# Kernel optimization log

Measured on AMD Instinct MI355X. Metric: run time of the kernel, lower is better.

The kernel has to match this reference:

```python
import jax, jax.numpy as jnp
import numpy as np

EPS_L2 = 1e-6   # featureL2Norm epsilon
EPS_MM = 1e-5   # MutualMatching epsilon
K_POOL = 2      # relocalization_k_size


def feature_l2norm(f):
    # torch: f / sqrt(sum(f^2, dim=1) + eps)
    norm = jnp.sqrt(jnp.sum(f * f, axis=1, keepdims=True) + EPS_L2)
    return f / norm


def mutual_matching(c):
    # c: [b, 1, f1, f2, f3, f4]
    b_max = jnp.max(c, axis=(2, 3), keepdims=True)  # max over source positions
    a_max = jnp.max(c, axis=(4, 5), keepdims=True)  # max over target positions
    return c * (c / (a_max + EPS_MM)) * (c / (b_max + EPS_MM))


def maxpool4d_max(c, k):
    # c: [b, 1, H, W, H2, W2] -> strided 4D max pool (max over all k^4 offsets)
    b = c.shape[0]
    H, W, H2, W2 = c.shape[2:]
    x = c[:, 0].reshape(b, H // k, k, W // k, k, H2 // k, k, W2 // k, k)
    x = x.transpose(0, 1, 3, 5, 7, 2, 4, 6, 8)
    x = x.reshape(b, H // k, W // k, H2 // k, W2 // k, k ** 4)
    return jnp.max(x, axis=-1)[:, None]  # [b,1,H/k,W/k,H2/k,W2/k]


def conv4d(x, w, b):
    # x: [N, Cin, d1, d2, d3, d4], w: [Cout, Cin, 3,3,3,3], SAME padding (pre-pad 1)
    y = jax.lax.conv_general_dilated(x, w, window_strides=(1, 1, 1, 1), padding='SAME')
    return y + b.reshape(1, -1, 1, 1, 1, 1)


def setup_inputs() -> dict:
    key = jax.random.key(0)
    ks = jax.random.split(key, 8)
    B, C, H, W = 8, 1024, 48, 48
    return {
        'feature_A': jax.random.normal(ks[0], (B, C, H, W), dtype=jnp.float32),
        'feature_B': jax.random.normal(ks[1], (B, C, H, W), dtype=jnp.float32),
        'w1': jax.random.normal(ks[2], (10, 1, 3, 3, 3, 3), dtype=jnp.float32) * 0.05,
        'b1': jnp.zeros((10,), dtype=jnp.float32),
        'w2': jax.random.normal(ks[3], (10, 10, 3, 3, 3, 3), dtype=jnp.float32) * 0.05,
        'b2': jnp.zeros((10,), dtype=jnp.float32),
        'w3': jax.random.normal(ks[4], (1, 10, 3, 3, 3, 3), dtype=jnp.float32) * 0.05,
        'b3': jnp.zeros((1,), dtype=jnp.float32),
    }


def reference(feature_A, feature_B, w1, b1, w2, b2, w3, b3):
    # 1) L2-normalize features over channels
    fa = feature_l2norm(feature_A)
    fb = feature_l2norm(feature_B)
    b, c, h, w = fa.shape
    # 2) 4D correlation: [b, hA*wA, hB*wB]
    corr = jnp.einsum('bcp,bcq->bpq', fa.reshape(b, c, h * w), fb.reshape(b, c, h * w))
    corr = corr.reshape(b, 1, h, w, h, w)
    # ReLU + featureL2Norm over singleton channel dim => x / sqrt(x^2 + eps)
    corr = jax.nn.relu(corr)
    corr = corr / jnp.sqrt(corr * corr + EPS_L2)
    # 3) strided 4D max pool (relocalization)
    corr = maxpool4d_max(corr, K_POOL)
    # 4) mutual matching
    corr = mutual_matching(corr)
    x = jax.nn.relu(conv4d(corr, w1, b1))
    x = jax.nn.relu(conv4d(x, w2, b2))
    x = jax.nn.relu(conv4d(x, w3, b3))
    # 6) mutual matching again
    return mutual_matching(x)
```

## Files before the change

kernel.cpp:

```cpp
#include <hip/hip_runtime.h>
#include <hip/hip_bf16.h>
#include <math.h>

#define C_   1024
#define P_   2304
#define S4   331776

typedef __attribute__((ext_vector_type(8))) short short8;
typedef __attribute__((ext_vector_type(4))) float f32x4;
typedef __attribute__((ext_vector_type(4))) unsigned int u32x4;

__device__ inline unsigned short f2bf(float v) {
  unsigned u = __builtin_bit_cast(unsigned, v);
  u += 0x7fffu + ((u >> 16) & 1u);
  return (unsigned short)(u >> 16);
}
__device__ inline float bf2f(unsigned short h) {
  unsigned u = ((unsigned)h) << 16;
  return __builtin_bit_cast(float, u);
}

__device__ inline void async16(const void* g, void* l) {
  __builtin_amdgcn_global_load_lds(
      (const __attribute__((address_space(1))) unsigned int*)g,
      (__attribute__((address_space(3))) unsigned int*)l, 16, 0, 0);
}

__global__ __launch_bounds__(256) void k_prep(
    const float* __restrict__ fA, const float* __restrict__ fB,
    unsigned short* __restrict__ TAhi, unsigned short* __restrict__ TAlo,
    unsigned short* __restrict__ TBhi, unsigned short* __restrict__ TBlo,
    float* __restrict__ part) {
  __shared__ float ld[64 * 65];
  __shared__ float pslds[512];
  const int c0 = blockIdx.x * 64, p0 = blockIdx.y * 64;
  const int fb = blockIdx.z, f = fb >> 3, b = fb & 7;
  const float* src = (f ? fB : fA) + (size_t)b * C_ * P_;
  unsigned short* Thi = (f ? TBhi : TAhi) + (size_t)b * P_ * C_;
  unsigned short* Tlo = (f ? TBlo : TAlo) + (size_t)b * P_ * C_;
  const int t = threadIdx.x;
#pragma unroll
  for (int e = 0; e < 4; ++e) {
    int cid = t + e * 256;
    int r = cid >> 4, ch = cid & 15;
    float4 v = *(const float4*)&src[(size_t)(c0 + r) * P_ + p0 + ch * 4];
    ld[r * 65 + ch * 4 + 0] = v.x;
    ld[r * 65 + ch * 4 + 1] = v.y;
    ld[r * 65 + ch * 4 + 2] = v.z;
    ld[r * 65 + ch * 4 + 3] = v.w;
  }
  __syncthreads();
#pragma unroll
  for (int e = 0; e < 2; ++e) {
    int ocid = t + e * 256;
    int pl = ocid >> 3, c8 = ocid & 7;
    unsigned short hi[8], lo[8];
    float sq = 0.f;
#pragma unroll
    for (int s = 0; s < 8; ++s) {
      float v = ld[(c8 * 8 + s) * 65 + pl];
      unsigned short h = f2bf(v);
      float rem = v - bf2f(h);
      hi[s] = h; lo[s] = f2bf(rem);
      sq = fmaf(v, v, sq);
    }
    size_t go = (size_t)(p0 + pl) * C_ + c0 + c8 * 8;
    *(uint4*)&Thi[go] = *(uint4*)hi;
    *(uint4*)&Tlo[go] = *(uint4*)lo;
    pslds[ocid] = sq;
  }
  __syncthreads();
  if (t < 64) {
    float s = 0.f;
#pragma unroll
    for (int c8 = 0; c8 < 8; ++c8) s += pslds[t * 8 + c8];
    part[((size_t)fb * 16 + blockIdx.x) * P_ + p0 + t] = s;
  }
}

__global__ void k_invnorm(const float* __restrict__ part, float* __restrict__ inv) {
  int p = blockIdx.x * 256 + threadIdx.x;
  int fb = blockIdx.y;
  float s = 1e-6f;
  for (int ct = 0; ct < 16; ++ct) s += part[((size_t)fb * 16 + ct) * P_ + p];
  inv[(size_t)fb * P_ + p] = 1.0f / sqrtf(s);
}

__global__ __launch_bounds__(256, 3) void k_corr_mfma(
    const unsigned short* __restrict__ TAhi_, const unsigned short* __restrict__ TAlo_,
    const unsigned short* __restrict__ TBhi_, const unsigned short* __restrict__ TBlo_,
    const float* __restrict__ invn, float* __restrict__ pooled) {
  __shared__ __align__(16) char lds_raw[37248];
  unsigned short* stage = (unsigned short*)lds_raw;
  float* epi = (float*)lds_raw;

  const int b = blockIdx.y;
  const size_t tb = (size_t)b * P_ * C_;
  const unsigned short* TAhi = TAhi_ + tb;
  const unsigned short* TAlo = TAlo_ + tb;
  const unsigned short* TBhi = TBhi_ + tb;
  const unsigned short* TBlo = TBlo_ + tb;
  float* out = pooled + (size_t)b * S4;

  const int g = blockIdx.x;
  const int xcd = g & 7, idx = g >> 3;
  const int ti = (xcd & 3) * 6 + idx % 6;
  const int tj = (xcd >> 2) * 12 + idx / 6;
  const int p0 = ti * 96, q0 = tj * 96;
  const int t = threadIdx.x;
  const int lane = t & 63, w = t >> 6;
  const int wr = w >> 1, wc = w & 1;
  const int m15 = lane & 15, q4 = lane >> 4;
  const int koff = q4 * 8;

  f32x4 acc[3][3];
#pragma unroll
  for (int a = 0; a < 3; ++a)
#pragma unroll
    for (int c = 0; c < 3; ++c) acc[a][c] = (f32x4){0.f, 0.f, 0.f, 0.f};

  const unsigned short* gld[8];
  int ldsb[8];
#pragma unroll
  for (int e = 0; e < 8; ++e) {
    int chunk = (w * 8 + e) * 64 + lane;
    int arr = chunk / 480;
    int rem = chunk - arr * 480;
    int row = rem / 5, kc = rem - row * 5;
    bool dum = (arr >= 4) || (kc == 4);
    if (arr >= 4) { arr = 0; row = 0; }
    const unsigned short* base = (arr == 0) ? TAhi : (arr == 1) ? TAlo
                               : (arr == 2) ? TBhi : TBlo;
    int pb = (arr < 2) ? p0 : q0;
    gld[e] = base + (size_t)(pb + row) * C_ + (dum ? 0 : kc * 8);
    ldsb[e] = (w * 8 + e) * 1024;
  }

  for (int kt = 0; kt < C_; kt += 32) {
    __syncthreads();
#pragma unroll
    for (int e = 0; e < 8; ++e)
      async16(gld[e] + kt, lds_raw + ldsb[e]);
    asm volatile("s_waitcnt vmcnt(0)" ::: "memory");
    __syncthreads();

    const unsigned short* Ah = stage;
    const unsigned short* Al = stage + 3840;
    const unsigned short* Bh = stage + 7680;
    const unsigned short* Bl = stage + 11520;
    short8 ah[3], al[3], bh[3], bl[3];
#pragma unroll
    for (int a = 0; a < 3; ++a) {
      int row = wr * 48 + a * 16 + m15;
      ah[a] = *(const short8*)&Ah[row * 40 + koff];
      al[a] = *(const short8*)&Al[row * 40 + koff];
    }
#pragma unroll
    for (int c = 0; c < 3; ++c) {
      int row = wc * 48 + c * 16 + m15;
      bh[c] = *(const short8*)&Bh[row * 40 + koff];
      bl[c] = *(const short8*)&Bl[row * 40 + koff];
    }
#pragma unroll
    for (int a = 0; a < 3; ++a)
#pragma unroll
      for (int c = 0; c < 3; ++c)
        acc[a][c] = __builtin_amdgcn_mfma_f32_16x16x32_bf16(ah[a], bh[c], acc[a][c], 0, 0, 0);
#pragma unroll
    for (int a = 0; a < 3; ++a)
#pragma unroll
      for (int c = 0; c < 3; ++c)
        acc[a][c] = __builtin_amdgcn_mfma_f32_16x16x32_bf16(ah[a], bl[c], acc[a][c], 0, 0, 0);
#pragma unroll
    for (int a = 0; a < 3; ++a)
#pragma unroll
      for (int c = 0; c < 3; ++c)
        acc[a][c] = __builtin_amdgcn_mfma_f32_16x16x32_bf16(al[a], bh[c], acc[a][c], 0, 0, 0);
  }
  __syncthreads();

  const float* invA = invn + (size_t)b * P_;
  const float* invB = invn + (size_t)(8 + b) * P_;
  float ib[3];
#pragma unroll
  for (int c = 0; c < 3; ++c) ib[c] = invB[q0 + wc * 48 + c * 16 + m15];
#pragma unroll
  for (int a = 0; a < 3; ++a) {
#pragma unroll
    for (int reg = 0; reg < 4; ++reg) {
      int pl = wr * 48 + a * 16 + q4 * 4 + reg;
      float ia = invA[p0 + pl];
#pragma unroll
      for (int c = 0; c < 3; ++c) {
        int ql = wc * 48 + c * 16 + m15;
        epi[pl * 97 + ql] = acc[a][c][reg] * ia * ib[c];
      }
    }
  }
  __syncthreads();

  for (int idx2 = t; idx2 < 576; idx2 += 256) {
    int j = idx2 / 24, l = idx2 % 24;
    float m = -1e30f;
#pragma unroll
    for (int dh = 0; dh < 2; ++dh)
#pragma unroll
      for (int dw = 0; dw < 2; ++dw) {
        int row = dh * 48 + 2 * j + dw;
#pragma unroll
        for (int d2 = 0; d2 < 2; ++d2)
#pragma unroll
          for (int dw2 = 0; dw2 < 2; ++dw2)
            m = fmaxf(m, epi[row * 97 + d2 * 48 + 2 * l + dw2]);
      }
    float r = fmaxf(m, 0.f);
    float v = r / sqrtf(r * r + 1e-6f);
    out[(size_t)(ti * 24 + j) * 576 + tj * 24 + l] = v;
  }
}

__global__ void k_rowmax(const float* __restrict__ x, float* __restrict__ amax) {
  int row = blockIdx.x;
  const float* r = x + (size_t)row * 576;
  float m = -1e30f;
  for (int e = threadIdx.x; e < 576; e += 64) m = fmaxf(m, r[e]);
  for (int off = 32; off > 0; off >>= 1) m = fmaxf(m, __shfl_down(m, off, 64));
  if (threadIdx.x == 0) amax[row] = m;
}

__global__ void k_colmax(const float* __restrict__ x, float* __restrict__ bmax) {
  __shared__ float pl[4][64];
  int b = blockIdx.x, klc = blockIdx.y * 64;
  int t = threadIdx.x;
  int kl = klc + (t & 63), seg = t >> 6;
  const float* xb = x + (size_t)b * S4;
  float m = -1e30f;
  for (int ij = seg * 144; ij < (seg + 1) * 144; ++ij)
    m = fmaxf(m, xb[(size_t)ij * 576 + kl]);
  pl[seg][t & 63] = m;
  __syncthreads();
  if (t < 64) {
    float r = fmaxf(fmaxf(pl[0][t], pl[1][t]), fmaxf(pl[2][t], pl[3][t]));
    bmax[b * 576 + klc + t] = r;
  }
}

__global__ void k_mm_apply(const float* __restrict__ x,
                           const float* __restrict__ amax,
                           const float* __restrict__ bmax,
                           float* __restrict__ y) {
  int i = blockIdx.x * 256 + threadIdx.x;
  int b = i / S4, r = i % S4;
  int ij = r / 576, kl = r % 576;
  float c = x[i];
  y[i] = c * (c / (amax[b * 576 + ij] + 1e-5f)) * (c / (bmax[b * 576 + kl] + 1e-5f));
}

__global__ __launch_bounds__(192, 4) void k_conv1_pack(
    const float* __restrict__ x, const float* __restrict__ w,
    const float* __restrict__ bias, unsigned int* __restrict__ C1p) {
  __shared__ float tile[9 * 702];
  const float* xb = x + (size_t)S4 * blockIdx.y;
  unsigned int* yb = C1p + ((size_t)blockIdx.y * 576 + blockIdx.x) * 6912;
  const int ij = blockIdx.x;
  const int i = ij / 24, j = ij % 24;
  const int t = threadIdx.x;
  const int k = t >> 3;
  const int l0 = (t & 7) * 3;

  if (t < 152) yb[6760 + t] = 0u;
  if (t < 100) {
    int kk, ll;
    if (t < 26)      { kk = 0;          ll = t; }
    else if (t < 52) { kk = 25;         ll = t - 26; }
    else if (t < 76) { kk = t - 52 + 1; ll = 0; }
    else             { kk = t - 76 + 1; ll = 25; }
    unsigned int* p = yb + (kk * 26 + ll) * 10;
#pragma unroll
    for (int q = 0; q < 10; ++q) p[q] = 0u;
  }

  int soff[4]; bool eok[4], klok[4]; int eidx[4];
#pragma unroll
  for (int q = 0; q < 4; ++q) {
    int e = t + q * 192;
    eidx[q] = e; eok[q] = (e < 702);
    int row = e / 27, col = e % 27;
    klok[q] = (row >= 1 && row < 25 && col >= 1 && col < 25);
    soff[q] = (row - 1) * 24 + (col - 1);
  }

  float acc[10][3];
#pragma unroll
  for (int co = 0; co < 10; ++co)
#pragma unroll
    for (int oo = 0; oo < 3; ++oo) acc[co][oo] = 0.f;

#pragma unroll
  for (int pln = 0; pln < 9; ++pln) {
    int ii = i + pln / 3 - 1, jj = j + pln % 3 - 1;
    const bool slab_ok = (ii >= 0 && ii < 24 && jj >= 0 && jj < 24);
    const float* src = xb + (size_t)(ii * 24 + jj) * 576;
#pragma unroll
    for (int q = 0; q < 4; ++q) {
      if (eok[q]) {
        float v = 0.f;
        if (slab_ok && klok[q]) v = src[soff[q]];
        tile[pln * 702 + eidx[q]] = v;
      }
    }
  }
  __syncthreads();
#pragma unroll
  for (int pln = 0; pln < 9; ++pln) {
    const float* base = &tile[pln * 702 + k * 27 + l0];
#pragma unroll
    for (int dk = 0; dk < 3; ++dk) {
      float c0 = base[dk * 27 + 0], c1 = base[dk * 27 + 1],
            c2 = base[dk * 27 + 2], c3 = base[dk * 27 + 3],
            c4 = base[dk * 27 + 4];
#pragma unroll
      for (int co = 0; co < 10; ++co) {
        const float* wr = w + (size_t)co * 81 + pln * 9 + dk * 3;
        float w0 = wr[0], w1 = wr[1], w2v = wr[2];
        acc[co][0] = fmaf(w0, c0, acc[co][0]);
        acc[co][0] = fmaf(w1, c1, acc[co][0]);
        acc[co][0] = fmaf(w2v, c2, acc[co][0]);
        acc[co][1] = fmaf(w0, c1, acc[co][1]);
        acc[co][1] = fmaf(w1, c2, acc[co][1]);
        acc[co][1] = fmaf(w2v, c3, acc[co][1]);
        acc[co][2] = fmaf(w0, c2, acc[co][2]);
        acc[co][2] = fmaf(w1, c3, acc[co][2]);
        acc[co][2] = fmaf(w2v, c4, acc[co][2]);
      }
    }
  }
#pragma unroll
  for (int oo = 0; oo < 3; ++oo) {
    unsigned int* baseo = yb + ((k + 1) * 26 + (l0 + oo + 1)) * 10;
#pragma unroll
    for (int co = 0; co < 10; ++co) {
      float v = fmaxf(acc[co][oo] + bias[co], 0.f);
      unsigned short hi = f2bf(v);
      unsigned short lo = f2bf(v - bf2f(hi));
      baseo[co] = ((unsigned)hi << 16) | (unsigned)lo;
    }
  }
}

__global__ void k_packw2(const float* __restrict__ w2,
                         unsigned short* __restrict__ Bh,
                         unsigned short* __restrict__ Bl) {
  int idx = blockIdx.x * 256 + threadIdx.x;
  if (idx >= 15360) return;
  int tap = idx >> 9;
  int n = (idx >> 5) & 15;
  int kap = idx & 31;
  float v = 0.f;
  if (tap < 27 && n < 10 && kap < 30) {
    int ci = kap % 10, dl = kap / 10;
    v = w2[(size_t)(n * 10 + ci) * 81 + tap * 3 + dl];
  }
  unsigned short hi = f2bf(v);
  unsigned short lo = f2bf(v - bf2f(hi));
  Bh[idx] = hi; Bl[idx] = lo;
}

__global__ void k_packw3(const float* __restrict__ w3,
                         unsigned short* __restrict__ Bh,
                         unsigned short* __restrict__ Bl) {
  int idx = blockIdx.x * 256 + threadIdx.x;
  if (idx >= 4608) return;
  int s = idx >> 9;
  int n = (idx >> 5) & 15;
  int kap = idx & 31;
  float v = 0.f;
  if (n < 3 && kap < 30) {
    int ci = kap % 10, dl = kap / 10;
    v = w3[(size_t)ci * 81 + s * 9 + n * 3 + dl];
  }
  unsigned short hi = f2bf(v);
  unsigned short lo = f2bf(v - bf2f(hi));
  Bh[idx] = hi; Bl[idx] = lo;
}

__global__ __launch_bounds__(256, 2) void k_conv2_mfma(
    const unsigned int* __restrict__ C1p,
    const unsigned short* __restrict__ Bh, const unsigned short* __restrict__ Bl,
    const float* __restrict__ bias, unsigned int* __restrict__ C2p) {
  __shared__ __align__(16) unsigned int lds[2 * 7168];
  const int b = blockIdx.y, ij = blockIdx.x;
  const int i = ij / 24, j = ij % 24;
  const int t = threadIdx.x, lane = t & 63, w = t >> 6;
  const int m15 = lane & 15, q4 = lane >> 4;

  unsigned int* yb = C2p + ((size_t)b * 576 + ij) * 6912;
  if (t < 152) yb[6760 + t] = 0u;
  if (t < 100) {
    int kk, ll;
    if (t < 26)      { kk = 0;          ll = t; }
    else if (t < 52) { kk = 25;         ll = t - 26; }
    else if (t < 76) { kk = t - 52 + 1; ll = 0; }
    else             { kk = t - 76 + 1; ll = 25; }
    unsigned int* p = yb + (kk * 26 + ll) * 10;
#pragma unroll
    for (int q = 0; q < 10; ++q) p[q] = 0u;
  }

  int rowb[9];
#pragma unroll
  for (int mi = 0; mi < 9; ++mi) {
    int kl = (w * 9 + mi) * 16 + m15;
    int kk = kl / 24, ll = kl % 24;
    rowb[mi] = ((kk + 1) * 26 + ll) * 10;
  }

  const unsigned int* sptr[9]; int tb[9];
#pragma unroll
  for (int s = 0; s < 9; ++s) {
    int di = s / 3 - 1, dj = s % 3 - 1;
    int ii = i + di, jj = j + dj;
    bool v = ((unsigned)ii < 24u) && ((unsigned)jj < 24u);
    sptr[s] = C1p + ((size_t)b * 576 + (size_t)(v ? (ii * 24 + jj) : ij)) * 6912;
    tb[s] = v ? s * 3 : 27;
  }

  auto STAGE = [&](const unsigned int* sp, int par) {
#pragma unroll
    for (int r = 0; r < 7; ++r) {
      const int g = w * 7 + r;
      const unsigned int* gp = sp + (g < 27 ? g * 256 : 0) + lane * 4;
      async16(gp, (char*)lds + par * 28672 + g * 1024);
    }
  };

  f32x4 acc[9];
#pragma unroll
  for (int mi = 0; mi < 9; ++mi) acc[mi] = (f32x4){0.f, 0.f, 0.f, 0.f};

  STAGE(sptr[0], 0);

#pragma unroll
  for (int s = 0; s < 9; ++s) {
    const int par = s & 1;
    short8 bh_[3], bl_[3];
#pragma unroll
    for (int dk = 0; dk < 3; ++dk) {
      size_t o = (size_t)((tb[s] + dk) * 16 + m15) * 32 + (size_t)q4 * 8;
      bh_[dk] = *(const short8*)(Bh + o);
      bl_[dk] = *(const short8*)(Bl + o);
    }
    if (s < 8) {
      STAGE(sptr[s + 1], par ^ 1);
      asm volatile("s_waitcnt vmcnt(13)" ::: "memory");
    } else {
      asm volatile("s_waitcnt vmcnt(6)" ::: "memory");
    }
    __builtin_amdgcn_s_barrier();
    __builtin_amdgcn_sched_barrier(0);

    const unsigned int* buf = lds + par * 7168;
#pragma unroll
    for (int dk = 0; dk < 3; ++dk) {
#pragma unroll
      for (int mi = 0; mi < 9; ++mi) {
        const uint2* p = (const uint2*)(buf + (rowb[mi] + (dk - 1) * 260 + q4 * 8));
        uint2 d0 = p[0], d1 = p[1], d2 = p[2], d3 = p[3];
        u32x4 hd, lv;
        hd.x = __builtin_amdgcn_perm(d0.y, d0.x, 0x07060302u);
        hd.y = __builtin_amdgcn_perm(d1.y, d1.x, 0x07060302u);
        hd.z = __builtin_amdgcn_perm(d2.y, d2.x, 0x07060302u);
        hd.w = __builtin_amdgcn_perm(d3.y, d3.x, 0x07060302u);
        lv.x = __builtin_amdgcn_perm(d0.y, d0.x, 0x05040100u);
        lv.y = __builtin_amdgcn_perm(d1.y, d1.x, 0x05040100u);
        lv.z = __builtin_amdgcn_perm(d2.y, d2.x, 0x05040100u);
        lv.w = __builtin_amdgcn_perm(d3.y, d3.x, 0x05040100u);
        short8 ah = __builtin_bit_cast(short8, hd);
        short8 al = __builtin_bit_cast(short8, lv);
        acc[mi] = __builtin_amdgcn_mfma_f32_16x16x32_bf16(ah, bh_[dk], acc[mi], 0, 0, 0);
        acc[mi] = __builtin_amdgcn_mfma_f32_16x16x32_bf16(ah, bl_[dk], acc[mi], 0, 0, 0);
        acc[mi] = __builtin_amdgcn_mfma_f32_16x16x32_bf16(al, bh_[dk], acc[mi], 0, 0, 0);
      }
    }
    __builtin_amdgcn_sched_barrier(0);
    __builtin_amdgcn_s_barrier();
  }

  if (m15 < 10) {
    const float bv = bias[m15];
#pragma unroll
    for (int mi = 0; mi < 9; ++mi) {
#pragma unroll
      for (int reg = 0; reg < 4; ++reg) {
        int kl = (w * 9 + mi) * 16 + q4 * 4 + reg;
        int kk = kl / 24 + 1, ll = kl % 24 + 1;
        float v = fmaxf(acc[mi][reg] + bv, 0.f);
        unsigned short hi = f2bf(v);
        unsigned short lo = f2bf(v - bf2f(hi));
        yb[(kk * 26 + ll) * 10 + m15] = ((unsigned)hi << 16) | (unsigned)lo;
      }
    }
  }
}

__global__ __launch_bounds__(256, 2) void k_conv3_mfma(
    const unsigned int* __restrict__ C2p,
    const unsigned short* __restrict__ Bh, const unsigned short* __restrict__ Bl,
    const float* __restrict__ bias, float* __restrict__ C3) {
  __shared__ __align__(16) unsigned int lds[2 * 7168];
  const int b = blockIdx.y, ij = blockIdx.x;
  const int i = ij / 24, j = ij % 24;
  const int t = threadIdx.x, lane = t & 63, w = t >> 6;
  const int m15 = lane & 15, q4 = lane >> 4;

  int rowb[10];
#pragma unroll
  for (int mi = 0; mi < 10; ++mi) {
    int m = (w * 10 + mi) * 16 + m15;
    int kp = m / 24, l = m % 24;
    rowb[mi] = (m < 624) ? (kp * 26 + l) * 10 : 0;
  }

  bool sval[9];
  const unsigned int* sptr[9];
#pragma unroll
  for (int s = 0; s < 9; ++s) {
    int di = s / 3 - 1, dj = s % 3 - 1;
    int ii = i + di, jj = j + dj;
    bool v = ((unsigned)ii < 24u) && ((unsigned)jj < 24u);
    sval[s] = v;
    sptr[s] = C2p + ((size_t)b * 576 + (size_t)(v ? (ii * 24 + jj) : ij)) * 6912;
  }

  short8 BHk[9], BLk[9];
#pragma unroll
  for (int s = 0; s < 9; ++s) {
    size_t o = (size_t)(s * 16 + m15) * 32 + (size_t)q4 * 8;
    BHk[s] = *(const short8*)(Bh + o);
    BLk[s] = *(const short8*)(Bl + o);
  }

  auto STAGE = [&](const unsigned int* sp, int par) {
#pragma unroll
    for (int r = 0; r < 7; ++r) {
      const int g = w * 7 + r;
      const unsigned int* gp = sp + (g < 27 ? g * 256 : 0) + lane * 4;
      async16(gp, (char*)lds + par * 28672 + g * 1024);
    }
  };

  f32x4 acc[10];
#pragma unroll
  for (int mi = 0; mi < 10; ++mi) acc[mi] = (f32x4){0.f, 0.f, 0.f, 0.f};

  STAGE(sptr[0], 0);

#pragma unroll
  for (int s = 0; s < 9; ++s) {
    const int par = s & 1;
    if (s < 8) {
      STAGE(sptr[s + 1], par ^ 1);
      asm volatile("s_waitcnt vmcnt(7)" ::: "memory");
    } else {
      asm volatile("s_waitcnt vmcnt(0)" ::: "memory");
    }
    __builtin_amdgcn_s_barrier();
    __builtin_amdgcn_sched_barrier(0);
    if (sval[s]) {
      const unsigned int* buf = lds + par * 7168;
#pragma unroll
      for (int mi = 0; mi < 10; ++mi) {
        const uint2* p = (const uint2*)(buf + rowb[mi] + q4 * 8);
        uint2 d0 = p[0], d1 = p[1], d2 = p[2], d3 = p[3];
        u32x4 hd, lv;
        hd.x = __builtin_amdgcn_perm(d0.y, d0.x, 0x07060302u);
        hd.y = __builtin_amdgcn_perm(d1.y, d1.x, 0x07060302u);
        hd.z = __builtin_amdgcn_perm(d2.y, d2.x, 0x07060302u);
        hd.w = __builtin_amdgcn_perm(d3.y, d3.x, 0x07060302u);
        lv.x = __builtin_amdgcn_perm(d0.y, d0.x, 0x05040100u);
        lv.y = __builtin_amdgcn_perm(d1.y, d1.x, 0x05040100u);
        lv.z = __builtin_amdgcn_perm(d2.y, d2.x, 0x05040100u);
        lv.w = __builtin_amdgcn_perm(d3.y, d3.x, 0x05040100u);
        short8 ah = __builtin_bit_cast(short8, hd);
        short8 al = __builtin_bit_cast(short8, lv);
        acc[mi] = __builtin_amdgcn_mfma_f32_16x16x32_bf16(ah, BHk[s], acc[mi], 0, 0, 0);
        acc[mi] = __builtin_amdgcn_mfma_f32_16x16x32_bf16(ah, BLk[s], acc[mi], 0, 0, 0);
        acc[mi] = __builtin_amdgcn_mfma_f32_16x16x32_bf16(al, BHk[s], acc[mi], 0, 0, 0);
      }
    }
    __builtin_amdgcn_sched_barrier(0);
    __builtin_amdgcn_s_barrier();
  }

  float* u = (float*)lds;
  if (m15 < 3) {
#pragma unroll
    for (int mi = 0; mi < 10; ++mi)
#pragma unroll
      for (int reg = 0; reg < 4; ++reg) {
        int m = (w * 10 + mi) * 16 + q4 * 4 + reg;
        u[m * 4 + m15] = acc[mi][reg];
      }
  }
  __syncthreads();
  const float bv = bias[0];
  float* outp = C3 + (size_t)b * S4 + (size_t)ij * 576;
  for (int idx = t; idx < 576; idx += 256) {
    int k = idx / 24, l = idx % 24;
    float sum = u[((k + 0) * 24 + l) * 4 + 0]
              + u[((k + 1) * 24 + l) * 4 + 1]
              + u[((k + 2) * 24 + l) * 4 + 2];
    outp[idx] = fmaxf(sum + bv, 0.f);
  }
}

extern "C" void kernel_launch(void* const* d_in, const int* in_sizes, int n_in,
                              void* d_out, int out_size, void* d_ws, size_t ws_size,
                              hipStream_t stream) {
  const float* fA = (const float*)d_in[0];
  const float* fB = (const float*)d_in[1];
  const float* w1 = (const float*)d_in[2];
  const float* b1 = (const float*)d_in[3];
  const float* w2 = (const float*)d_in[4];
  const float* b2 = (const float*)d_in[5];
  const float* w3 = (const float*)d_in[6];
  const float* b3 = (const float*)d_in[7];
  float* out = (float*)d_out;
  float* ws = (float*)d_ws;
  (void)in_sizes; (void)n_in; (void)out_size; (void)ws_size;

  unsigned int* C1p  = (unsigned int*)ws;
  unsigned int* C2p  = (unsigned int*)(ws + 31850496);
  unsigned short* TAhi = (unsigned short*)ws;
  unsigned short* TAlo = TAhi + (size_t)8 * P_ * C_;
  unsigned short* TBhi = TAlo + (size_t)8 * P_ * C_;
  unsigned short* TBlo = TBhi + (size_t)8 * P_ * C_;
  float* pooled = ws + 37748736;
  float* part   = ws + 40402944;
  float* invn   = ws + 40992768;
  float* amax1  = ws + 41029632;
  float* bmax1  = ws + 41034240;
  float* C3     = ws + 0;
  float* amax2  = ws + 2654208;
  float* bmax2  = ws + 2658816;
  unsigned short* Bh2 = (unsigned short*)(ws + 63700992);
  unsigned short* Bl2 = Bh2 + 15360;
  unsigned short* Bh3 = Bl2 + 15360;
  unsigned short* Bl3 = Bh3 + 4608;

  k_prep<<<dim3(16, 36, 16), 256, 0, stream>>>(fA, fB, TAhi, TAlo, TBhi, TBlo, part);
  k_invnorm<<<dim3(9, 16), 256, 0, stream>>>(part, invn);
  k_corr_mfma<<<dim3(576, 8), 256, 0, stream>>>(TAhi, TAlo, TBhi, TBlo, invn, pooled);

  k_rowmax<<<dim3(8 * 576), 64, 0, stream>>>(pooled, amax1);
  k_colmax<<<dim3(8, 9), 256, 0, stream>>>(pooled, bmax1);
  k_mm_apply<<<dim3(10368), 256, 0, stream>>>(pooled, amax1, bmax1, pooled);

  k_packw2<<<dim3(60), 256, 0, stream>>>(w2, Bh2, Bl2);
  k_packw3<<<dim3(18), 256, 0, stream>>>(w3, Bh3, Bl3);
  k_conv1_pack<<<dim3(576, 8), 192, 0, stream>>>(pooled, w1, b1, C1p);
  k_conv2_mfma<<<dim3(576, 8), 256, 0, stream>>>(C1p, Bh2, Bl2, b2, C2p);
  k_conv3_mfma<<<dim3(576, 8), 256, 0, stream>>>(C2p, Bh3, Bl3, b3, C3);

  k_rowmax<<<dim3(8 * 576), 64, 0, stream>>>(C3, amax2);
  k_colmax<<<dim3(8, 9), 256, 0, stream>>>(C3, bmax2);
  k_mm_apply<<<dim3(10368), 256, 0, stream>>>(C3, amax2, bmax2, out);
}
```

Baseline: 1.060 ms.

## Enlarge correlation tile to 192x96 with swizzled LDS and in-register pooling

The correlation GEMM tile grows from 96x96 to 192x96 (each wave computes 6x3 MFMA tiles), halving the grid and raising B-operand reuse per staged K slice. Padded LDS rows are replaced by an XOR-swizzled 64-byte row layout to avoid bank conflicts without wasted space. The epilogue now does part of the 2x2x2x2 max pool in registers with lane shuffles before writing a compacted LDS buffer. The trade-offs are higher accumulator register pressure, which may cut occupancy, and fewer blocks to spread across CUs.

```diff
diff --git a/kernel.cpp b/kernel.cpp
--- a/kernel.cpp
+++ b/kernel.cpp
@@ -90,8 +90,7 @@
     const unsigned short* __restrict__ TAhi_, const unsigned short* __restrict__ TAlo_,
     const unsigned short* __restrict__ TBhi_, const unsigned short* __restrict__ TBlo_,
     const float* __restrict__ invn, float* __restrict__ pooled) {
-  __shared__ __align__(16) char lds_raw[37248];
-  unsigned short* stage = (unsigned short*)lds_raw;
+  __shared__ __align__(16) char lds_raw[36864];
   float* epi = (float*)lds_raw;
 
   const int b = blockIdx.y;
@@ -104,118 +103,113 @@
 
   const int g = blockIdx.x;
   const int xcd = g & 7, idx = g >> 3;
-  const int ti = (xcd & 3) * 6 + idx % 6;
-  const int tj = (xcd >> 2) * 12 + idx / 6;
-  const int p0 = ti * 96, q0 = tj * 96;
+  const int ti = (xcd & 1) * 6 + idx % 6;
+  const int tj = (xcd >> 1) * 6 + idx / 6;
+  const int p0 = ti * 192, q0 = tj * 96;
   const int t = threadIdx.x;
   const int lane = t & 63, w = t >> 6;
   const int wr = w >> 1, wc = w & 1;
   const int m15 = lane & 15, q4 = lane >> 4;
-  const int koff = q4 * 8;
-
-  f32x4 acc[3][3];
-#pragma unroll
-  for (int a = 0; a < 3; ++a)
+  const int laneoff = (q4 ^ ((m15 >> 1) & 3)) * 16;
+
+  f32x4 acc[6][3];
+#pragma unroll
+  for (int a = 0; a < 6; ++a)
 #pragma unroll
     for (int c = 0; c < 3; ++c) acc[a][c] = (f32x4){0.f, 0.f, 0.f, 0.f};
 
-  const unsigned short* gld[8];
-  int ldsb[8];
-#pragma unroll
-  for (int e = 0; e < 8; ++e) {
-    int chunk = (w * 8 + e) * 64 + lane;
-    int arr = chunk / 480;
-    int rem = chunk - arr * 480;
-    int row = rem / 5, kc = rem - row * 5;
-    bool dum = (arr >= 4) || (kc == 4);
-    if (arr >= 4) { arr = 0; row = 0; }
-    const unsigned short* base = (arr == 0) ? TAhi : (arr == 1) ? TAlo
-                               : (arr == 2) ? TBhi : TBlo;
-    int pb = (arr < 2) ? p0 : q0;
-    gld[e] = base + (size_t)(pb + row) * C_ + (dum ? 0 : kc * 8);
-    ldsb[e] = (w * 8 + e) * 1024;
-  }
+  const unsigned short* gld[9];
+  int ldsb[9];
+#pragma unroll
+  for (int e = 0; e < 9; ++e) {
+    int chunk = (w * 9 + e) * 64 + lane;
+    int row = chunk >> 2, cpos = chunk & 3;
+    int cglob = cpos ^ ((row >> 1) & 3);
+    const unsigned short* bp; int roff;
+    if (row < 192)      { bp = TAhi; roff = p0 + row; }
+    else if (row < 384) { bp = TAlo; roff = p0 + row - 192; }
+    else if (row < 480) { bp = TBhi; roff = q0 + row - 384; }
+    else                { bp = TBlo; roff = q0 + row - 480; }
+    gld[e] = bp + (size_t)roff * C_ + cglob * 8;
+    ldsb[e] = (w * 9 + e) * 1024;
+  }
+
+  auto STAGE = [&](int kt) {
+#pragma unroll
+    for (int e = 0; e < 9; ++e)
+      async16(gld[e] + kt, lds_raw + ldsb[e]);
+  };
 
   for (int kt = 0; kt < C_; kt += 32) {
     __syncthreads();
-#pragma unroll
-    for (int e = 0; e < 8; ++e)
-      async16(gld[e] + kt, lds_raw + ldsb[e]);
+    STAGE(kt);
     asm volatile("s_waitcnt vmcnt(0)" ::: "memory");
     __syncthreads();
 
-    const unsigned short* Ah = stage;
-    const unsigned short* Al = stage + 3840;
-    const unsigned short* Bh = stage + 7680;
-    const unsigned short* Bl = stage + 11520;
-    short8 ah[3], al[3], bh[3], bl[3];
-#pragma unroll
-    for (int a = 0; a < 3; ++a) {
-      int row = wr * 48 + a * 16 + m15;
-      ah[a] = *(const short8*)&Ah[row * 40 + koff];
-      al[a] = *(const short8*)&Al[row * 40 + koff];
-    }
+    const char* buf = lds_raw;
+    short8 bh[3], bl[3];
 #pragma unroll
     for (int c = 0; c < 3; ++c) {
-      int row = wc * 48 + c * 16 + m15;
-      bh[c] = *(const short8*)&Bh[row * 40 + koff];
-      bl[c] = *(const short8*)&Bl[row * 40 + koff];
-    }
-#pragma unroll
-    for (int a = 0; a < 3; ++a)
+      int rB = (384 + wc * 48 + c * 16 + m15) * 64;
+      bh[c] = *(const short8*)(buf + rB + laneoff);
+      bl[c] = *(const short8*)(buf + rB + 6144 + laneoff);
+    }
+#pragma unroll
+    for (int a = 0; a < 6; ++a) {
+      int rA = (wr * 96 + a * 16 + m15) * 64;
+      short8 ah = *(const short8*)(buf + rA + laneoff);
+      short8 al = *(const short8*)(buf + rA + 12288 + laneoff);
 #pragma unroll
       for (int c = 0; c < 3; ++c)
-        acc[a][c] = __builtin_amdgcn_mfma_f32_16x16x32_bf16(ah[a], bh[c], acc[a][c], 0, 0, 0);
-#pragma unroll
-    for (int a = 0; a < 3; ++a)
+        acc[a][c] = __builtin_amdgcn_mfma_f32_16x16x32_bf16(ah, bh[c], acc[a][c], 0, 0, 0);
 #pragma unroll
       for (int c = 0; c < 3; ++c)
-        acc[a][c] = __builtin_amdgcn_mfma_f32_16x16x32_bf16(ah[a], bl[c], acc[a][c], 0, 0, 0);
-#pragma unroll
-    for (int a = 0; a < 3; ++a)
+        acc[a][c] = __builtin_amdgcn_mfma_f32_16x16x32_bf16(ah, bl[c], acc[a][c], 0, 0, 0);
 #pragma unroll
       for (int c = 0; c < 3; ++c)
-        acc[a][c] = __builtin_amdgcn_mfma_f32_16x16x32_bf16(al[a], bh[c], acc[a][c], 0, 0, 0);
+        acc[a][c] = __builtin_amdgcn_mfma_f32_16x16x32_bf16(al, bh[c], acc[a][c], 0, 0, 0);
+    }
   }
   __syncthreads();
 
   const float* invA = invn + (size_t)b * P_;
   const float* invB = invn + (size_t)(8 + b) * P_;
-  float ib[3];
-#pragma unroll
-  for (int c = 0; c < 3; ++c) ib[c] = invB[q0 + wc * 48 + c * 16 + m15];
-#pragma unroll
-  for (int a = 0; a < 3; ++a) {
-#pragma unroll
-    for (int reg = 0; reg < 4; ++reg) {
-      int pl = wr * 48 + a * 16 + q4 * 4 + reg;
-      float ia = invA[p0 + pl];
-#pragma unroll
-      for (int c = 0; c < 3; ++c) {
-        int ql = wc * 48 + c * 16 + m15;
-        epi[pl * 97 + ql] = acc[a][c][reg] * ia * ib[c];
+  float ibv[3];
+#pragma unroll
+  for (int c = 0; c < 3; ++c) ibv[c] = invB[q0 + wc * 48 + c * 16 + m15];
+#pragma unroll
+  for (int a = 0; a < 6; ++a) {
+    float4 ia = *(const float4*)&invA[p0 + wr * 96 + a * 16 + q4 * 4];
+    int h_local = wr * 2 + (a >= 3 ? 1 : 0);
+    int wbase = (a % 3) * 8 + q4 * 2;
+#pragma unroll
+    for (int c = 0; c < 3; ++c) {
+      float v0 = acc[a][c][0] * ia.x * ibv[c];
+      float v1 = acc[a][c][1] * ia.y * ibv[c];
+      float v2 = acc[a][c][2] * ia.z * ibv[c];
+      float v3 = acc[a][c][3] * ia.w * ibv[c];
+      float m0 = fmaxf(v0, v1), m1 = fmaxf(v2, v3);
+      m0 = fmaxf(m0, __shfl_xor(m0, 1, 64));
+      m1 = fmaxf(m1, __shfl_xor(m1, 1, 64));
+      if (!(m15 & 1)) {
+        int ql2 = wc * 24 + c * 8 + (m15 >> 1);
+        epi[(h_local * 24 + wbase + 0) * 50 + ql2] = m0;
+        epi[(h_local * 24 + wbase + 1) * 50 + ql2] = m1;
       }
     }
   }
   __syncthreads();
 
-  for (int idx2 = t; idx2 < 576; idx2 += 256) {
-    int j = idx2 / 24, l = idx2 % 24;
-    float m = -1e30f;
-#pragma unroll
-    for (int dh = 0; dh < 2; ++dh)
-#pragma unroll
-      for (int dw = 0; dw < 2; ++dw) {
-        int row = dh * 48 + 2 * j + dw;
-#pragma unroll
-        for (int d2 = 0; d2 < 2; ++d2)
-#pragma unroll
-          for (int dw2 = 0; dw2 < 2; ++dw2)
-            m = fmaxf(m, epi[row * 97 + d2 * 48 + 2 * l + dw2]);
-      }
+  for (int ix = t; ix < 1152; ix += 256) {
+    int orow = ix / 24, ocol = ix % 24;
+    int dlt = orow / 24, wp = orow % 24;
+    const float* r0 = &epi[((dlt * 2 + 0) * 24 + wp) * 50];
+    const float* r1 = &epi[((dlt * 2 + 1) * 24 + wp) * 50];
+    float m = fmaxf(fmaxf(r0[ocol], r0[24 + ocol]),
+                    fmaxf(r1[ocol], r1[24 + ocol]));
     float r = fmaxf(m, 0.f);
     float v = r / sqrtf(r * r + 1e-6f);
-    out[(size_t)(ti * 24 + j) * 576 + tj * 24 + l] = v;
+    out[(size_t)(ti * 48 + orow) * 576 + tj * 24 + ocol] = v;
   }
 }
 
@@ -650,7 +644,7 @@
 
   k_prep<<<dim3(16, 36, 16), 256, 0, stream>>>(fA, fB, TAhi, TAlo, TBhi, TBlo, part);
   k_invnorm<<<dim3(9, 16), 256, 0, stream>>>(part, invn);
-  k_corr_mfma<<<dim3(576, 8), 256, 0, stream>>>(TAhi, TAlo, TBhi, TBlo, invn, pooled);
+  k_corr_mfma<<<dim3(288, 8), 256, 0, stream>>>(TAhi, TAlo, TBhi, TBlo, invn, pooled);
 
   k_rowmax<<<dim3(8 * 576), 64, 0, stream>>>(pooled, amax1);
   k_colmax<<<dim3(8, 9), 256, 0, stream>>>(pooled, bmax1);
```

Result: faster. 992.8 us (-6.3%).
